# Kernel tuning notes

Measured on AMD Instinct MI355X. Metric: run time of the kernel, lower is better.

The kernel has to match this reference:

```python
import jax, jax.numpy as jnp
import numpy as np

B, T, E = 64, 1024, 2048  # BATCH_SIZE, TRAIN_LEN, EMBEDDING_LEN (E > T branch, as in repo configs)


def setup_inputs() -> dict:
    key = jax.random.key(0)
    delay_embedding = jax.random.normal(key, (B, T, E), dtype=jnp.float32)
    return {"delay_embedding": delay_embedding}


def reference(delay_embedding):
    """Hankel anti-diagonal segmented mean (embedding_2_predict_y, all_y=False).

    delay_embedding: [B, T, E]. Elements with equal index-sum s = i + j lie on the
    same anti-diagonal; the torch code averages each such diagonal. With
    all_y=False it returns diagonals s = T .. T+E-2  ->  output shape [B, E-1].
    One fused segment_sum pass replaces the per-batch, per-diagonal python loops.
    """
    Bv, Tv, Ev = delay_embedding.shape
    S = Tv + Ev - 1  # number of anti-diagonals
    seg = (jnp.arange(Tv)[:, None] + jnp.arange(Ev)[None, :]).reshape(-1)  # [T*E]
    data = delay_embedding.reshape(Bv, Tv * Ev).T  # [T*E, B], segments on axis 0
    sums = jax.ops.segment_sum(data, seg, num_segments=S)  # [S, B]
    counts = jax.ops.segment_sum(jnp.ones((Tv * Ev,), jnp.float32), seg, num_segments=S)  # [S]
    means = (sums / counts[:, None]).T  # [B, S]
    return means[:, Tv:]  # [B, E-1]
```

## Files before the change

### kernel.cpp

```cpp
#include <hip/hip_runtime.h>


#define T_LEN 1024
#define E_LEN 2048
#define K_OUT (E_LEN - 1)
#define B_SZ  64
#define NZ    4
#define ROWS  (T_LEN / NZ)
#define TPB   128
#define NBLK  (NZ * B_SZ * 4)

__global__ void __launch_bounds__(TPB)
diag_accum(const float* __restrict__ in, float* __restrict__ out) {
    const int bid  = blockIdx.x;
    const int zraw = bid & (NZ - 1);
    const int b    = (bid >> 2) & (B_SZ - 1);
    const int x    = bid >> 8;

    int z = zraw;
    if (x == 3) z = (zraw < 2) ? (3 - zraw) : (zraw - 2);

    const int g  = x * TPB + threadIdx.x;
    const int k0 = g << 2;
    const int r0 = z * ROWS;
    const int r1 = r0 + ROWS;

    const int il0 = max(r0, k0     - (T_LEN - 1));
    const int il3 = max(r0, k0 + 3 - (T_LEN - 1));
    if (il0 >= r1) return;

    const float* p = in + (size_t)b * T_LEN * E_LEN
                        + (size_t)il0 * (E_LEN - 1)
                        + (size_t)(T_LEN + k0);
    float sx = 0.f, sy = 0.f, sz = 0.f, sw = 0.f;
    int i = il0;

    const int head_end = min(il3, r1);
    for (; i < head_end; ++i) {
        sx += p[0];
        if (i >= k0 + 1 - (T_LEN - 1)) sy += p[1];
        if (i >= k0 + 2 - (T_LEN - 1)) sz += p[2];
        p += (E_LEN - 1);
    }

    #pragma unroll 8
    for (; i < r1; ++i) {
        float v[4];
        __builtin_memcpy(v, p, 16);
        sx += v[0]; sy += v[1]; sz += v[2]; sw += v[3];
        p += (E_LEN - 1);
    }

    const int ov = k0 - (T_LEN - 1);
    const float n0 = (float)(T_LEN - max(0, ov));
    const float n1 = (float)(T_LEN - max(0, ov + 1));
    const float n2 = (float)(T_LEN - max(0, ov + 2));
    float* o = out + (size_t)b * K_OUT + k0;
    atomicAdd(o + 0, sx * (1.0f / n0));
    atomicAdd(o + 1, sy * (1.0f / n1));
    atomicAdd(o + 2, sz * (1.0f / n2));
    if (k0 + 3 < K_OUT) {
        const float n3 = (float)(T_LEN - max(0, ov + 3));
        atomicAdd(o + 3, sw * (1.0f / n3));
    }
}

extern "C" void kernel_launch(void* const* d_in, const int* in_sizes, int n_in,
                              void* d_out, int out_size, void* d_ws, size_t ws_size,
                              hipStream_t stream) {
    const float* in = (const float*)d_in[0];
    float* out = (float*)d_out;

    hipMemsetAsync(out, 0, sizeof(float) * B_SZ * K_OUT, stream);

    diag_accum<<<NBLK, TPB, 0, stream>>>(in, out);
}
```

Baseline: 94.65 us.

## Split diagonal work into 64-row chunks with trimmed block map

Reworks the grid decomposition so each block handles 256 output columns over a 64-row chunk, instead of 512 columns over a quarter of the rows. The block-to-work map enumerates only (column group, row chunk) pairs that hold valid anti-diagonal elements, so the upper column groups get fewer blocks and little work is wasted on early-exit threads. The aim is better load balance and more blocks in flight on the GPU. The cost is more atomicAdds per output and smaller 64-thread blocks.

Measured after the change: 103.7 us. 1.1x slower.

```diff
diff --git a/kernel.cpp b/kernel.cpp
--- a/kernel.cpp
+++ b/kernel.cpp
@@ -5,25 +5,30 @@
 #define E_LEN 2048
 #define K_OUT (E_LEN - 1)
 #define B_SZ  64
-#define NZ    4
-#define ROWS  (T_LEN / NZ)
-#define TPB   128
-#define NBLK  (NZ * B_SZ * 4)
+#define RCH   64
+#define UPB   104
+#define NBLK  (UPB * B_SZ)
 
-__global__ void __launch_bounds__(TPB)
+__global__ void __launch_bounds__(64)
 diag_accum(const float* __restrict__ in, float* __restrict__ out) {
-    const int bid  = blockIdx.x;
-    const int zraw = bid & (NZ - 1);
-    const int b    = (bid >> 2) & (B_SZ - 1);
-    const int x    = bid >> 8;
+    const int b = blockIdx.x & (B_SZ - 1);
+    const int u = blockIdx.x >> 6;
 
-    int z = zraw;
-    if (x == 3) z = (zraw < 2) ? (3 - zraw) : (zraw - 2);
+    int G, rc;
+    if (u < 64) {
+        G = u >> 4;
+        rc = u & 15;
+    } else {
+        const int t = u - 64;
+        if (t < 16)      { G = 4; rc = t;      }
+        else if (t < 28) { G = 5; rc = t - 12; }
+        else if (t < 36) { G = 6; rc = t - 20; }
+        else             { G = 7; rc = t - 24; }
+    }
 
-    const int g  = x * TPB + threadIdx.x;
-    const int k0 = g << 2;
-    const int r0 = z * ROWS;
-    const int r1 = r0 + ROWS;
+    const int k0 = G * 256 + (threadIdx.x << 2);
+    const int r0 = rc * RCH;
+    const int r1 = r0 + RCH;
 
     const int il0 = max(r0, k0     - (T_LEN - 1));
     const int il3 = max(r0, k0 + 3 - (T_LEN - 1));
@@ -73,5 +78,5 @@
 
     hipMemsetAsync(out, 0, sizeof(float) * B_SZ * K_OUT, stream);
 
-    diag_accum<<<NBLK, TPB, 0, stream>>>(in, out);
+    diag_accum<<<NBLK, 64, 0, stream>>>(in, out);
 }
```

## Restructure work split into 256-thread blocks with shared-memory pre-reduction before atomics

Applied to the files above, without the earlier changes.

Reorganizes the grid so each 256-thread block covers a 512-column group and two 64-row chunks, with waves pairing up on row chunks. Per-thread partial sums are combined in shared memory before global atomics, which halves the atomic traffic. It also switches to unsafeAtomicAdd, which may map to hardware float atomics. Grid shape and load balance change, and blocks in the triangular region may have idle waves.

New measurement: 86.03 us. 1.1x faster.

```diff
diff --git a/kernel.cpp b/kernel.cpp
--- a/kernel.cpp
+++ b/kernel.cpp
@@ -5,63 +5,69 @@
 #define E_LEN 2048
 #define K_OUT (E_LEN - 1)
 #define B_SZ  64
-#define NZ    4
-#define ROWS  (T_LEN / NZ)
-#define TPB   128
-#define NBLK  (NZ * B_SZ * 4)
+#define NBLK  (28 * B_SZ)
 
-__global__ void __launch_bounds__(TPB)
+__global__ void __launch_bounds__(256)
 diag_accum(const float* __restrict__ in, float* __restrict__ out) {
-    const int bid  = blockIdx.x;
-    const int zraw = bid & (NZ - 1);
-    const int b    = (bid >> 2) & (B_SZ - 1);
-    const int x    = bid >> 8;
+    __shared__ float lacc[1024];
 
-    int z = zraw;
-    if (x == 3) z = (zraw < 2) ? (3 - zraw) : (zraw - 2);
+    const int b  = blockIdx.x & (B_SZ - 1);
+    const int u2 = blockIdx.x >> 6;
 
-    const int g  = x * TPB + threadIdx.x;
-    const int k0 = g << 2;
-    const int r0 = z * ROWS;
-    const int r1 = r0 + ROWS;
+    int G, rcb;
+    if (u2 < 8)       { G = 0; rcb = u2 * 2;            }
+    else if (u2 < 16) { G = 1; rcb = (u2 - 8) * 2;      }
+    else if (u2 < 24) { G = 2; rcb = (u2 - 16) * 2;     }
+    else              { G = 3; rcb = 8 + (u2 - 24) * 2; }
 
-    const int il0 = max(r0, k0     - (T_LEN - 1));
+    const int w    = threadIdx.x >> 6;
+    const int lane = threadIdx.x & 63;
+    const int rc   = rcb + (w >> 1);
+    const int p    = w & 1;
+
+    const int k0 = G * 512 + p * 256 + (lane << 2);
+    const int r0 = rc * 64;
+    const int r1 = r0 + 64;
+
+    int il0       = max(r0, k0     - (T_LEN - 1));
     const int il3 = max(r0, k0 + 3 - (T_LEN - 1));
-    if (il0 >= r1) return;
 
-    const float* p = in + (size_t)b * T_LEN * E_LEN
-                        + (size_t)il0 * (E_LEN - 1)
-                        + (size_t)(T_LEN + k0);
     float sx = 0.f, sy = 0.f, sz = 0.f, sw = 0.f;
-    int i = il0;
+    if (il0 < r1) {
+        const float* pp = in + (size_t)b * T_LEN * E_LEN
+                             + (size_t)il0 * (E_LEN - 1)
+                             + (size_t)(T_LEN + k0);
+        int i = il0;
 
-    const int head_end = min(il3, r1);
-    for (; i < head_end; ++i) {
-        sx += p[0];
-        if (i >= k0 + 1 - (T_LEN - 1)) sy += p[1];
-        if (i >= k0 + 2 - (T_LEN - 1)) sz += p[2];
-        p += (E_LEN - 1);
+        const int head_end = min(il3, r1);
+        for (; i < head_end; ++i) {
+            sx += pp[0];
+            if (i >= k0 + 1 - (T_LEN - 1)) sy += pp[1];
+            if (i >= k0 + 2 - (T_LEN - 1)) sz += pp[2];
+            pp += (E_LEN - 1);
+        }
+
+        #pragma unroll 8
+        for (; i < r1; ++i) {
+            float v[4];
+            __builtin_memcpy(v, pp, 16);
+            sx += v[0]; sy += v[1]; sz += v[2]; sw += v[3];
+            pp += (E_LEN - 1);
+        }
     }
 
-    #pragma unroll 8
-    for (; i < r1; ++i) {
-        float v[4];
-        __builtin_memcpy(v, p, 16);
-        sx += v[0]; sy += v[1]; sz += v[2]; sw += v[3];
-        p += (E_LEN - 1);
-    }
+    float4* dst = (float4*)&lacc[w * 256 + (lane << 2)];
+    *dst = make_float4(sx, sy, sz, sw);
+    __syncthreads();
 
-    const int ov = k0 - (T_LEN - 1);
-    const float n0 = (float)(T_LEN - max(0, ov));
-    const float n1 = (float)(T_LEN - max(0, ov + 1));
-    const float n2 = (float)(T_LEN - max(0, ov + 2));
-    float* o = out + (size_t)b * K_OUT + k0;
-    atomicAdd(o + 0, sx * (1.0f / n0));
-    atomicAdd(o + 1, sy * (1.0f / n1));
-    atomicAdd(o + 2, sz * (1.0f / n2));
-    if (k0 + 3 < K_OUT) {
-        const float n3 = (float)(T_LEN - max(0, ov + 3));
-        atomicAdd(o + 3, sw * (1.0f / n3));
+    #pragma unroll 2
+    for (int t = threadIdx.x; t < 512; t += 256) {
+        const int k = G * 512 + t;
+        if (k < K_OUT) {
+            const float v = lacc[t] + lacc[512 + t];
+            const int cnt = T_LEN - max(0, k - (T_LEN - 1));
+            unsafeAtomicAdd(&out[(size_t)b * K_OUT + k], v * (1.0f / (float)cnt));
+        }
     }
 }
 
@@ -73,5 +79,5 @@
 
     hipMemsetAsync(out, 0, sizeof(float) * B_SZ * K_OUT, stream);
 
-    diag_accum<<<NBLK, TPB, 0, stream>>>(in, out);
+    diag_accum<<<NBLK, 256, 0, stream>>>(in, out);
 }
```
